# Performance work log

Hardware: AMD Instinct MI355X
Metric: run time of the kernel (lower is better)

## Reference

```python
import jax, jax.numpy as jnp
import numpy as np

D_MODEL = 1024
N_HEADS = 16
HEAD_DIM = D_MODEL // N_HEADS  # 64
LATENT = 256
B, S = 2, 2048


def setup_inputs() -> dict:
    key = jax.random.key(0)
    ks = jax.random.split(key, 13)
    sc = 0.02
    inp = {
        'x': jax.random.normal(ks[0], (B, S, D_MODEL), jnp.float32),
        'Wq': jax.random.normal(ks[1], (D_MODEL, D_MODEL), jnp.float32) * sc,
        'bq': jnp.zeros((D_MODEL,), jnp.float32),
        'Wkd': jax.random.normal(ks[2], (D_MODEL, LATENT), jnp.float32) * sc,
        'bkd': jnp.zeros((LATENT,), jnp.float32),
        'Wvd': jax.random.normal(ks[3], (D_MODEL, LATENT), jnp.float32) * sc,
        'bvd': jnp.zeros((LATENT,), jnp.float32),
        'Wku': jax.random.normal(ks[4], (LATENT, D_MODEL), jnp.float32) * sc,
        'bku': jnp.zeros((D_MODEL,), jnp.float32),
        'Wvu': jax.random.normal(ks[5], (LATENT, D_MODEL), jnp.float32) * sc,
        'bvu': jnp.zeros((D_MODEL,), jnp.float32),
        'Wo': jax.random.normal(ks[6], (D_MODEL, D_MODEL), jnp.float32) * sc,
        'bo': jnp.zeros((D_MODEL,), jnp.float32),
    }
    return inp


def reference(x, Wq, bq, Wkd, bkd, Wvd, bvd, Wku, bku, Wvu, bvu, Wo, bo):
    b, s, _ = x.shape
    # projections
    Q = x @ Wq + bq                      # [b, s, d_model]
    K_latent = x @ Wkd + bkd             # [b, s, latent]
    V_latent = x @ Wvd + bvd             # [b, s, latent]
    K = K_latent @ Wku + bku             # [b, s, d_model]
    V = V_latent @ Wvu + bvu             # [b, s, d_model]
    # split heads
    Qh = Q.reshape(b, s, N_HEADS, HEAD_DIM)
    Kh = K.reshape(b, s, N_HEADS, HEAD_DIM)
    Vh = V.reshape(b, s, N_HEADS, HEAD_DIM)
    scale = 1.0 / jnp.sqrt(jnp.asarray(HEAD_DIM, x.dtype))
    scores = jnp.einsum('bqhd,bkhd->bhqk', Qh, Kh) * scale  # [b,h,s,s]
    attn = jax.nn.softmax(scores, axis=-1)
    ctx = jnp.einsum('bhqk,bkhd->bqhd', attn, Vh).reshape(b, s, D_MODEL)
    out = ctx @ Wo + bo
    return out
```

## Files before the change

kernel.cpp:

```cpp
#include <hip/hip_runtime.h>
#include <hip/hip_bf16.h>
#include <cstddef>

#define B_SZ 2
#define SEQ  2048
#define DM   1024
#define NH   16
#define HD   64
#define LAT  256
#define MTOT (B_SZ*SEQ)
#define NQKV 1536
#define QSCALE 0.18033688011112042f

typedef short bf16x8 __attribute__((ext_vector_type(8)));
typedef float floatx4 __attribute__((ext_vector_type(4)));
typedef unsigned short u16;

#if __has_builtin(__builtin_amdgcn_exp2f)
#define EXP2(x) __builtin_amdgcn_exp2f(x)
#else
#define EXP2(x) exp2f(x)
#endif

__device__ __forceinline__ u16 f2bf(float f) {
  union { float f; unsigned u; } a; a.f = f;
  unsigned r = a.u + 0x7FFFu + ((a.u >> 16) & 1u);
  return (u16)(r >> 16);
}

__device__ __forceinline__ floatx4 mfma16(bf16x8 a, bf16x8 b, floatx4 c) {
  return __builtin_amdgcn_mfma_f32_16x16x32_bf16(a, b, c, 0, 0, 0);
}

__device__ __forceinline__ void load16(const u16* g, u16* l) {
  __builtin_amdgcn_global_load_lds((const __attribute__((address_space(1))) unsigned*)g,
                                   (__attribute__((address_space(3))) unsigned*)l, 16, 0, 0);
}

__device__ void transpose_tile(const float* __restrict__ W, u16* __restrict__ WT,
                               int K, int N, int k0, int n0, u16 (*t)[65]) {
  const int r = threadIdx.x >> 4;
  const int c4 = (threadIdx.x & 15) * 4;
#pragma unroll
  for (int s = 0; s < 4; s++) {
    int row = s * 16 + r;
    float4 v = *(const float4*)&W[(size_t)(k0 + row) * N + n0 + c4];
    t[row][c4 + 0] = f2bf(v.x); t[row][c4 + 1] = f2bf(v.y);
    t[row][c4 + 2] = f2bf(v.z); t[row][c4 + 3] = f2bf(v.w);
  }
  __syncthreads();
  const int r2 = threadIdx.x >> 2;
  const int c8 = (threadIdx.x & 3) * 16;
  __align__(16) u16 tmp[16];
#pragma unroll
  for (int i = 0; i < 16; i++) tmp[i] = t[c8 + i][r2];
  u16* dst = WT + (size_t)(n0 + r2) * K + k0 + c8;
  *(bf16x8*)dst       = *(const bf16x8*)&tmp[0];
  *(bf16x8*)(dst + 8) = *(const bf16x8*)&tmp[8];
}

__global__ __launch_bounds__(256)
void prep_k(const float* __restrict__ x, u16* __restrict__ xb,
            const float* __restrict__ Wq, const float* __restrict__ Wkd,
            const float* __restrict__ Wvd, const float* __restrict__ Wku,
            const float* __restrict__ Wvu, const float* __restrict__ Wo,
            u16* __restrict__ WstkT, u16* __restrict__ WkuT,
            u16* __restrict__ WvuT, u16* __restrict__ WoT,
            const float* __restrict__ bq, const float* __restrict__ bkd,
            const float* __restrict__ bvd, float* __restrict__ bqkv) {
  __shared__ u16 t[64][65];
  const int blk = blockIdx.x;
  if (blk < 4096) {
    int i = blk * 256 + threadIdx.x;
    float4 v = ((const float4*)x)[i];
    ushort4 o; o.x = f2bf(v.x); o.y = f2bf(v.y); o.z = f2bf(v.z); o.w = f2bf(v.w);
    ((ushort4*)xb)[i] = o;
  } else if (blk < 4352) {
    int tt = blk - 4096;
    transpose_tile(Wq, WstkT, DM, DM, (tt >> 4) * 64, (tt & 15) * 64, t);
  } else if (blk < 4416) {
    int tt = blk - 4352;
    transpose_tile(Wkd, WstkT + (size_t)DM * DM, DM, LAT, (tt >> 2) * 64, (tt & 3) * 64, t);
  } else if (blk < 4480) {
    int tt = blk - 4416;
    transpose_tile(Wvd, WstkT + (size_t)1280 * DM, DM, LAT, (tt >> 2) * 64, (tt & 3) * 64, t);
  } else if (blk < 4544) {
    int tt = blk - 4480;
    transpose_tile(Wku, WkuT, LAT, DM, (tt >> 4) * 64, (tt & 15) * 64, t);
  } else if (blk < 4608) {
    int tt = blk - 4544;
    transpose_tile(Wvu, WvuT, LAT, DM, (tt >> 4) * 64, (tt & 15) * 64, t);
  } else if (blk < 4864) {
    int tt = blk - 4608;
    transpose_tile(Wo, WoT, DM, DM, (tt >> 4) * 64, (tt & 15) * 64, t);
  } else {
    int i = (blk - 4864) * 256 + threadIdx.x;
    float v = (i < 1024) ? bq[i] : (i < 1280) ? bkd[i - 1024] : bvd[i - 1280];
    bqkv[i] = v;
  }
}

template<int TM, int OUT_BF16, int VT1>
__global__ __launch_bounds__(256)
void gemm_bt(const u16* __restrict__ A0, const u16* __restrict__ A1,
             const u16* __restrict__ BT0, const u16* __restrict__ BT1,
             const float* __restrict__ bias0, const float* __restrict__ bias1,
             void* __restrict__ C0, void* __restrict__ C1,
             int M, int N, int Kd, int lda, float qscale, int qcols) {
  constexpr int FM = TM / 32;
  __shared__ u16 As[TM * 64];
  __shared__ u16 Bs[64 * 64];
  const u16* A  = blockIdx.z ? A1 : A0;
  const u16* BT = blockIdx.z ? BT1 : BT0;
  const float* bias = blockIdx.z ? bias1 : bias0;
  void* C = blockIdx.z ? C1 : C0;

  const int tid = threadIdx.x;
  const int m0 = blockIdx.y * TM, n0 = blockIdx.x * 64;
  const int wave = tid >> 6, lane = tid & 63;
  const int l15 = lane & 15, quad = lane >> 4;
  const int wm = (wave >> 1) * (TM / 2), wn = (wave & 1) * 32;

  floatx4 acc[FM][2];
#pragma unroll
  for (int i = 0; i < FM; i++)
#pragma unroll
    for (int j = 0; j < 2; j++) acc[i][j] = (floatx4){0.f, 0.f, 0.f, 0.f};

  const int tr = tid >> 3;
  const int tc8 = (tid & 7) * 8;
  const u16* Ag = A  + (size_t)(m0 + tr) * lda + tc8;
  const u16* Bg = BT + (size_t)(n0 + tr) * Kd + tc8;
  u16* AsW = &As[(size_t)tid * 8];
  u16* BsW = &Bs[(size_t)tid * 8];

  for (int k0 = 0; k0 < Kd; k0 += 64) {
    __syncthreads();
#pragma unroll
    for (int s = 0; s < FM; s++)
      load16(Ag + (size_t)(s * 32) * lda + k0, AsW + s * 2048);
#pragma unroll
    for (int s = 0; s < 2; s++)
      load16(Bg + (size_t)(s * 32) * Kd  + k0, BsW + s * 2048);
    __syncthreads();
#pragma unroll
    for (int kk = 0; kk < 2; kk++) {
      bf16x8 af[FM], bfr[2];
#pragma unroll
      for (int i = 0; i < FM; i++)
        af[i]  = *(const bf16x8*)&As[(wm + i * 16 + l15) * 64 + kk * 32 + quad * 8];
#pragma unroll
      for (int j = 0; j < 2; j++)
        bfr[j] = *(const bf16x8*)&Bs[(wn + j * 16 + l15) * 64 + kk * 32 + quad * 8];
#pragma unroll
      for (int i = 0; i < FM; i++)
#pragma unroll
        for (int j = 0; j < 2; j++)
          acc[i][j] = mfma16(af[i], bfr[j], acc[i][j]);
    }
  }

  if (VT1 && blockIdx.z == 1) {
#pragma unroll
    for (int i = 0; i < FM; i++) {
      int row = m0 + wm + i * 16 + quad * 4;
      int bb = row >> 11, sb = row & 2047;
#pragma unroll
      for (int j = 0; j < 2; j++) {
        int col = n0 + wn + j * 16 + l15;
        float bv = bias[col];
        union { u16 u[4]; uint2 w2; } tv;
#pragma unroll
        for (int r = 0; r < 4; r++) tv.u[r] = f2bf(acc[i][j][r] + bv);
        *(uint2*)((u16*)C + ((size_t)(bb * 16 + (col >> 6)) * 64 + (col & 63)) * SEQ + sb) = tv.w2;
      }
    }
  } else {
#pragma unroll
    for (int i = 0; i < FM; i++) {
      int row = m0 + wm + i * 16 + quad * 4;
#pragma unroll
      for (int j = 0; j < 2; j++) {
        int col = n0 + wn + j * 16 + l15;
        float bv = bias[col];
        float sc = (col < qcols) ? qscale : 1.f;
#pragma unroll
        for (int r = 0; r < 4; r++) {
          float v = (acc[i][j][r] + bv) * sc;
          if (OUT_BF16) ((u16*)C)[(size_t)(row + r) * N + col] = f2bf(v);
          else          ((float*)C)[(size_t)(row + r) * N + col] = v;
        }
      }
    }
  }
}

__global__ __launch_bounds__(256, 2)
void attn_fused(const u16* __restrict__ Q, const u16* __restrict__ K,
                const u16* __restrict__ VT, u16* __restrict__ CTX) {
  __shared__ float Ocmb[64][68];
  __shared__ float Lw[4][64];
  __shared__ u16 Plds[4][2][64][40];
  const int lin = blockIdx.y * gridDim.x + blockIdx.x;
  const int idx = lin >> 3;
  const int bh = (lin & 7) * 4 + (idx >> 5);
  const int q0 = (idx & 31) * 64;
  const int b = bh >> 4, h = bh & 15;
  const int wave = threadIdx.x >> 6, lane = threadIdx.x & 63;
  const int l15 = lane & 15, quad = lane >> 4;

  bf16x8 qf[4][2];
  {
    const u16* Qp = Q + (size_t)(b * SEQ + q0 + l15) * NQKV + h * HD + quad * 8;
#pragma unroll
    for (int qi = 0; qi < 4; qi++)
#pragma unroll
      for (int h2 = 0; h2 < 2; h2++)
        qf[qi][h2] = *(const bf16x8*)(Qp + (size_t)qi * 16 * NQKV + h2 * 32);
  }
  const u16* Kp = K + (size_t)(b * SEQ) * DM + h * HD + quad * 8;
  const u16* Vp = VT + ((size_t)bh * HD + l15) * SEQ + quad * 8;

  floatx4 o[4][4];
#pragma unroll
  for (int dt = 0; dt < 4; dt++)
#pragma unroll
    for (int qi = 0; qi < 4; qi++) o[dt][qi] = (floatx4){0.f, 0.f, 0.f, 0.f};
  float ls[4] = {0.f, 0.f, 0.f, 0.f};

  const int kb0 = wave * 512;

  bf16x8 kfb[2][2][2], vfb[2][4];
#pragma unroll
  for (int ki = 0; ki < 2; ki++)
#pragma unroll
    for (int h2 = 0; h2 < 2; h2++)
      kfb[0][ki][h2] = *(const bf16x8*)(Kp + (size_t)(kb0 + ki * 16 + l15) * DM + h2 * 32);
#pragma unroll
  for (int dt = 0; dt < 4; dt++)
    vfb[0][dt] = *(const bf16x8*)(Vp + (size_t)(dt * 16) * SEQ + kb0);

#pragma unroll 2
  for (int it = 0; it < 16; ++it) {
    const int cur = it & 1, nxt = cur ^ 1;
    const int kb = kb0 + it * 32;
    if (it < 15) {
      const int kn = kb + 32;
#pragma unroll
      for (int ki = 0; ki < 2; ki++)
#pragma unroll
        for (int h2 = 0; h2 < 2; h2++)
          kfb[nxt][ki][h2] = *(const bf16x8*)(Kp + (size_t)(kn + ki * 16 + l15) * DM + h2 * 32);
    }
    __builtin_amdgcn_s_setprio(1);
    if (it > 0) {
#pragma unroll
      for (int qi = 0; qi < 4; qi++) {
        bf16x8 pf = *(const bf16x8*)&Plds[wave][nxt][qi * 16 + l15][quad * 8];
#pragma unroll
        for (int dt = 0; dt < 4; dt++)
          o[dt][qi] = mfma16(vfb[nxt][dt], pf, o[dt][qi]);
      }
    }
    if (it < 15) {
      const int kn = kb + 32;
#pragma unroll
      for (int dt = 0; dt < 4; dt++)
        vfb[nxt][dt] = *(const bf16x8*)(Vp + (size_t)(dt * 16) * SEQ + kn);
    }
    unsigned pw[4][4];
#pragma unroll
    for (int qi = 0; qi < 4; qi++) {
#pragma unroll
      for (int ki = 0; ki < 2; ki++) {
        floatx4 z = (floatx4){0.f, 0.f, 0.f, 0.f};
        z = mfma16(kfb[cur][ki][0], qf[qi][0], z);
        z = mfma16(kfb[cur][ki][1], qf[qi][1], z);
        float p0 = EXP2(z[0]), p1 = EXP2(z[1]), p2 = EXP2(z[2]), p3 = EXP2(z[3]);
        ls[qi] += (p0 + p1) + (p2 + p3);
        unsigned u0 = __float_as_uint(p0) + 0x8000u;
        unsigned u1 = __float_as_uint(p1) + 0x8000u;
        unsigned u2 = __float_as_uint(p2) + 0x8000u;
        unsigned u3 = __float_as_uint(p3) + 0x8000u;
        pw[qi][ki * 2]     = __builtin_amdgcn_perm(u1, u0, 0x07060302u);
        pw[qi][ki * 2 + 1] = __builtin_amdgcn_perm(u3, u2, 0x07060302u);
      }
    }
    __builtin_amdgcn_s_setprio(0);
#pragma unroll
    for (int qi = 0; qi < 4; qi++) {
      uint2 w0; w0.x = pw[qi][0]; w0.y = pw[qi][1];
      *(uint2*)&Plds[wave][cur][qi * 16 + l15][quad * 4] = w0;
      uint2 w1; w1.x = pw[qi][2]; w1.y = pw[qi][3];
      *(uint2*)&Plds[wave][cur][qi * 16 + l15][16 + quad * 4] = w1;
    }
  }
  __builtin_amdgcn_s_setprio(1);
#pragma unroll
  for (int qi = 0; qi < 4; qi++) {
    bf16x8 pf = *(const bf16x8*)&Plds[wave][1][qi * 16 + l15][quad * 8];
#pragma unroll
    for (int dt = 0; dt < 4; dt++)
      o[dt][qi] = mfma16(vfb[1][dt], pf, o[dt][qi]);
  }
  __builtin_amdgcn_s_setprio(0);

#pragma unroll
  for (int qi = 0; qi < 4; qi++) {
    float v = ls[qi];
    v += __shfl_xor(v, 16);
    v += __shfl_xor(v, 32);
    if (quad == 0) Lw[wave][qi * 16 + l15] = v;
  }
  if (wave == 0) {
#pragma unroll
    for (int dt = 0; dt < 4; dt++)
#pragma unroll
      for (int qi = 0; qi < 4; qi++)
        *(floatx4*)&Ocmb[qi * 16 + l15][dt * 16 + quad * 4] = o[dt][qi];
  }
  __syncthreads();
  if (wave == 1) {
#pragma unroll
    for (int dt = 0; dt < 4; dt++)
#pragma unroll
      for (int qi = 0; qi < 4; qi++) {
        floatx4* pp = (floatx4*)&Ocmb[qi * 16 + l15][dt * 16 + quad * 4];
        *pp = *pp + o[dt][qi];
      }
  }
  __syncthreads();
  if (wave == 2) {
#pragma unroll
    for (int dt = 0; dt < 4; dt++)
#pragma unroll
      for (int qi = 0; qi < 4; qi++) {
        floatx4* pp = (floatx4*)&Ocmb[qi * 16 + l15][dt * 16 + quad * 4];
        *pp = *pp + o[dt][qi];
      }
  }
  __syncthreads();
  if (wave == 3) {
#pragma unroll
    for (int qi = 0; qi < 4; qi++) {
      int qq = qi * 16 + l15;
      float lt = Lw[0][qq] + Lw[1][qq] + Lw[2][qq] + Lw[3][qq];
      float inv = 1.f / lt;
      u16* Crow = CTX + (size_t)(b * SEQ + q0 + qq) * DM + h * HD + quad * 4;
#pragma unroll
      for (int dt = 0; dt < 4; dt++) {
        floatx4 ov = o[dt][qi] + *(const floatx4*)&Ocmb[qq][dt * 16 + quad * 4];
        union { u16 u[4]; uint2 w2; } tv;
#pragma unroll
        for (int r = 0; r < 4; r++) tv.u[r] = f2bf(ov[r] * inv);
        *(uint2*)(Crow + dt * 16) = tv.w2;
      }
    }
  }
}

extern "C" void kernel_launch(void* const* d_in, const int* in_sizes, int n_in,
                              void* d_out, int out_size, void* d_ws, size_t ws_size,
                              hipStream_t stream) {
  const float* x   = (const float*)d_in[0];
  const float* Wq  = (const float*)d_in[1];
  const float* bq  = (const float*)d_in[2];
  const float* Wkd = (const float*)d_in[3];
  const float* bkd = (const float*)d_in[4];
  const float* Wvd = (const float*)d_in[5];
  const float* bvd = (const float*)d_in[6];
  const float* Wku = (const float*)d_in[7];
  const float* bku = (const float*)d_in[8];
  const float* Wvu = (const float*)d_in[9];
  const float* bvu = (const float*)d_in[10];
  const float* Wo  = (const float*)d_in[11];
  const float* bo  = (const float*)d_in[12];
  float* out = (float*)d_out;

  float* bqkv = (float*)d_ws;
  u16* p = (u16*)((char*)d_ws + 1536 * sizeof(float));
  u16* xb    = p; p += (size_t)MTOT * DM;
  u16* WstkT = p; p += (size_t)NQKV * DM;
  u16* WkuT  = p; p += (size_t)DM * LAT;
  u16* WvuT  = p; p += (size_t)DM * LAT;
  u16* WoT   = p; p += (size_t)DM * DM;
  u16* QKVb  = p; p += (size_t)MTOT * NQKV;
  u16* Kb    = p; p += (size_t)MTOT * DM;
  u16* VTb   = p; p += (size_t)MTOT * DM;
  u16* CXb   = p; p += (size_t)MTOT * DM;

  prep_k<<<4870, 256, 0, stream>>>(x, xb, Wq, Wkd, Wvd, Wku, Wvu, Wo,
                                   WstkT, WkuT, WvuT, WoT, bq, bkd, bvd, bqkv);

  gemm_bt<128, 1, 0><<<dim3(NQKV / 64, MTOT / 128, 1), 256, 0, stream>>>(
      xb, xb, WstkT, WstkT, bqkv, bqkv, QKVb, QKVb, MTOT, NQKV, DM, DM, QSCALE, DM);
  gemm_bt<128, 1, 1><<<dim3(DM / 64, MTOT / 128, 2), 256, 0, stream>>>(
      QKVb + 1024, QKVb + 1280, WkuT, WvuT, bku, bvu, Kb, VTb, MTOT, DM, LAT, NQKV, 1.f, 0);

  attn_fused<<<dim3(SEQ / 64, B_SZ * NH), 256, 0, stream>>>(QKVb, Kb, VTb, CXb);

  gemm_bt<64, 0, 0><<<dim3(DM / 64, MTOT / 64, 1), 256, 0, stream>>>(
      CXb, CXb, WoT, WoT, bo, bo, out, out, MTOT, DM, DM, DM, 1.f, 0);
}
```

Before: 224.0 us.

## Switch attention to 32x32x16 MFMA and pass P via lane shuffles instead of LDS

Rewrites the attention inner loop to use 32x32x16 bf16 MFMA tiles instead of 16x16x32, with matching fragment layouts for Q, K, V^T and the output accumulators. The probability tile is now repacked into B-operand form with cross-half-wave shuffles, which removes the per-wave LDS staging buffer and its store/load round trip. The aim is fewer MFMA issues, no LDS traffic in the hot loop, and a lighter epilogue. The cost is extra shuffles and selects per tile, and P·V now runs in the same iteration as QK^T, so the previous software pipelining between them is gone.

```diff
diff --git a/kernel.cpp b/kernel.cpp
--- a/kernel.cpp
+++ b/kernel.cpp
@@ -14,6 +14,7 @@
 
 typedef short bf16x8 __attribute__((ext_vector_type(8)));
 typedef float floatx4 __attribute__((ext_vector_type(4)));
+typedef float floatx16 __attribute__((ext_vector_type(16)));
 typedef unsigned short u16;
 
 #if __has_builtin(__builtin_amdgcn_exp2f)
@@ -30,6 +31,10 @@
 
 __device__ __forceinline__ floatx4 mfma16(bf16x8 a, bf16x8 b, floatx4 c) {
   return __builtin_amdgcn_mfma_f32_16x16x32_bf16(a, b, c, 0, 0, 0);
+}
+
+__device__ __forceinline__ floatx16 mfma32(bf16x8 a, bf16x8 b, floatx16 c) {
+  return __builtin_amdgcn_mfma_f32_32x32x16_bf16(a, b, c, 0, 0, 0);
 }
 
 __device__ __forceinline__ void load16(const u16* g, u16* l) {
@@ -200,45 +205,46 @@
                 const u16* __restrict__ VT, u16* __restrict__ CTX) {
   __shared__ float Ocmb[64][68];
   __shared__ float Lw[4][64];
-  __shared__ u16 Plds[4][2][64][40];
   const int lin = blockIdx.y * gridDim.x + blockIdx.x;
   const int idx = lin >> 3;
   const int bh = (lin & 7) * 4 + (idx >> 5);
   const int q0 = (idx & 31) * 64;
   const int b = bh >> 4, h = bh & 15;
   const int wave = threadIdx.x >> 6, lane = threadIdx.x & 63;
-  const int l15 = lane & 15, quad = lane >> 4;
-
-  bf16x8 qf[4][2];
+  const int l31 = lane & 31;
+  const int hi = lane >> 5;
+
+  bf16x8 qf[2][4];
   {
-    const u16* Qp = Q + (size_t)(b * SEQ + q0 + l15) * NQKV + h * HD + quad * 8;
-#pragma unroll
-    for (int qi = 0; qi < 4; qi++)
-#pragma unroll
-      for (int h2 = 0; h2 < 2; h2++)
-        qf[qi][h2] = *(const bf16x8*)(Qp + (size_t)qi * 16 * NQKV + h2 * 32);
-  }
-  const u16* Kp = K + (size_t)(b * SEQ) * DM + h * HD + quad * 8;
-  const u16* Vp = VT + ((size_t)bh * HD + l15) * SEQ + quad * 8;
-
-  floatx4 o[4][4];
-#pragma unroll
-  for (int dt = 0; dt < 4; dt++)
-#pragma unroll
-    for (int qi = 0; qi < 4; qi++) o[dt][qi] = (floatx4){0.f, 0.f, 0.f, 0.f};
-  float ls[4] = {0.f, 0.f, 0.f, 0.f};
+    const u16* Qp = Q + (size_t)(b * SEQ + q0 + l31) * NQKV + h * HD + hi * 8;
+#pragma unroll
+    for (int qh = 0; qh < 2; qh++)
+#pragma unroll
+      for (int dc = 0; dc < 4; dc++)
+        qf[qh][dc] = *(const bf16x8*)(Qp + (size_t)(qh * 32) * NQKV + dc * 16);
+  }
+  const u16* Kp = K + ((size_t)(b * SEQ) + l31) * DM + h * HD + hi * 8;
+  const u16* Vp = VT + ((size_t)bh * HD + l31) * SEQ + hi * 8;
+
+  floatx16 o[2][2];
+  const floatx16 zf16 = {0.f,0.f,0.f,0.f,0.f,0.f,0.f,0.f,0.f,0.f,0.f,0.f,0.f,0.f,0.f,0.f};
+#pragma unroll
+  for (int dh = 0; dh < 2; dh++)
+#pragma unroll
+    for (int qh = 0; qh < 2; qh++) o[dh][qh] = zf16;
+  float ls[2] = {0.f, 0.f};
 
   const int kb0 = wave * 512;
 
-  bf16x8 kfb[2][2][2], vfb[2][4];
-#pragma unroll
-  for (int ki = 0; ki < 2; ki++)
-#pragma unroll
-    for (int h2 = 0; h2 < 2; h2++)
-      kfb[0][ki][h2] = *(const bf16x8*)(Kp + (size_t)(kb0 + ki * 16 + l15) * DM + h2 * 32);
-#pragma unroll
-  for (int dt = 0; dt < 4; dt++)
-    vfb[0][dt] = *(const bf16x8*)(Vp + (size_t)(dt * 16) * SEQ + kb0);
+  bf16x8 kfb[2][4], vfb[2][2][2];
+#pragma unroll
+  for (int dc = 0; dc < 4; dc++)
+    kfb[0][dc] = *(const bf16x8*)(Kp + (size_t)kb0 * DM + dc * 16);
+#pragma unroll
+  for (int dh = 0; dh < 2; dh++)
+#pragma unroll
+    for (int kh = 0; kh < 2; kh++)
+      vfb[0][dh][kh] = *(const bf16x8*)(Vp + (size_t)(dh * 32) * SEQ + kb0 + kh * 16);
 
 #pragma unroll 2
   for (int it = 0; it < 16; ++it) {
@@ -247,114 +253,121 @@
     if (it < 15) {
       const int kn = kb + 32;
 #pragma unroll
-      for (int ki = 0; ki < 2; ki++)
-#pragma unroll
-        for (int h2 = 0; h2 < 2; h2++)
-          kfb[nxt][ki][h2] = *(const bf16x8*)(Kp + (size_t)(kn + ki * 16 + l15) * DM + h2 * 32);
-    }
-    __builtin_amdgcn_s_setprio(1);
-    if (it > 0) {
-#pragma unroll
-      for (int qi = 0; qi < 4; qi++) {
-        bf16x8 pf = *(const bf16x8*)&Plds[wave][nxt][qi * 16 + l15][quad * 8];
-#pragma unroll
-        for (int dt = 0; dt < 4; dt++)
-          o[dt][qi] = mfma16(vfb[nxt][dt], pf, o[dt][qi]);
+      for (int dc = 0; dc < 4; dc++)
+        kfb[nxt][dc] = *(const bf16x8*)(Kp + (size_t)kn * DM + dc * 16);
+#pragma unroll
+      for (int dh = 0; dh < 2; dh++)
+#pragma unroll
+        for (int kh = 0; kh < 2; kh++)
+          vfb[nxt][dh][kh] = *(const bf16x8*)(Vp + (size_t)(dh * 32) * SEQ + kn + kh * 16);
+    }
+#pragma unroll
+    for (int qh = 0; qh < 2; qh++) {
+      floatx16 z = zf16;
+      __builtin_amdgcn_s_setprio(1);
+#pragma unroll
+      for (int dc = 0; dc < 4; dc++)
+        z = mfma32(kfb[cur][dc], qf[qh][dc], z);
+      __builtin_amdgcn_s_setprio(0);
+      float p[16];
+#pragma unroll
+      for (int r = 0; r < 16; r++) p[r] = EXP2(z[r]);
+      ls[qh] += (((p[0] + p[1]) + (p[2] + p[3])) + ((p[4] + p[5]) + (p[6] + p[7])))
+              + (((p[8] + p[9]) + (p[10] + p[11])) + ((p[12] + p[13]) + (p[14] + p[15])));
+      unsigned wt[8];
+#pragma unroll
+      for (int i = 0; i < 8; i++) {
+        unsigned ua = __float_as_uint(p[2 * i]) + 0x8000u;
+        unsigned ub = __float_as_uint(p[2 * i + 1]) + 0x8000u;
+        wt[i] = __builtin_amdgcn_perm(ub, ua, 0x07060302u);
       }
-    }
-    if (it < 15) {
-      const int kn = kb + 32;
-#pragma unroll
-      for (int dt = 0; dt < 4; dt++)
-        vfb[nxt][dt] = *(const bf16x8*)(Vp + (size_t)(dt * 16) * SEQ + kn);
-    }
-    unsigned pw[4][4];
-#pragma unroll
-    for (int qi = 0; qi < 4; qi++) {
-#pragma unroll
-      for (int ki = 0; ki < 2; ki++) {
-        floatx4 z = (floatx4){0.f, 0.f, 0.f, 0.f};
-        z = mfma16(kfb[cur][ki][0], qf[qi][0], z);
-        z = mfma16(kfb[cur][ki][1], qf[qi][1], z);
-        float p0 = EXP2(z[0]), p1 = EXP2(z[1]), p2 = EXP2(z[2]), p3 = EXP2(z[3]);
-        ls[qi] += (p0 + p1) + (p2 + p3);
-        unsigned u0 = __float_as_uint(p0) + 0x8000u;
-        unsigned u1 = __float_as_uint(p1) + 0x8000u;
-        unsigned u2 = __float_as_uint(p2) + 0x8000u;
-        unsigned u3 = __float_as_uint(p3) + 0x8000u;
-        pw[qi][ki * 2]     = __builtin_amdgcn_perm(u1, u0, 0x07060302u);
-        pw[qi][ki * 2 + 1] = __builtin_amdgcn_perm(u3, u2, 0x07060302u);
+      unsigned sx[8];
+#pragma unroll
+      for (int i = 0; i < 8; i++) sx[i] = (unsigned)__shfl_xor((int)wt[i], 32);
+      union { unsigned u[4]; bf16x8 v; } b0, b1;
+      b0.u[0] = hi ? sx[2] : wt[0];
+      b0.u[1] = hi ? sx[3] : wt[1];
+      b0.u[2] = hi ? wt[2] : sx[0];
+      b0.u[3] = hi ? wt[3] : sx[1];
+      b1.u[0] = hi ? sx[6] : wt[4];
+      b1.u[1] = hi ? sx[7] : wt[5];
+      b1.u[2] = hi ? wt[6] : sx[4];
+      b1.u[3] = hi ? wt[7] : sx[5];
+      __builtin_amdgcn_s_setprio(1);
+#pragma unroll
+      for (int dh = 0; dh < 2; dh++) {
+        o[dh][qh] = mfma32(vfb[cur][dh][0], b0.v, o[dh][qh]);
+        o[dh][qh] = mfma32(vfb[cur][dh][1], b1.v, o[dh][qh]);
       }
-    }
-    __builtin_amdgcn_s_setprio(0);
-#pragma unroll
-    for (int qi = 0; qi < 4; qi++) {
-      uint2 w0; w0.x = pw[qi][0]; w0.y = pw[qi][1];
-      *(uint2*)&Plds[wave][cur][qi * 16 + l15][quad * 4] = w0;
-      uint2 w1; w1.x = pw[qi][2]; w1.y = pw[qi][3];
-      *(uint2*)&Plds[wave][cur][qi * 16 + l15][16 + quad * 4] = w1;
-    }
-  }
-  __builtin_amdgcn_s_setprio(1);
-#pragma unroll
-  for (int qi = 0; qi < 4; qi++) {
-    bf16x8 pf = *(const bf16x8*)&Plds[wave][1][qi * 16 + l15][quad * 8];
-#pragma unroll
-    for (int dt = 0; dt < 4; dt++)
-      o[dt][qi] = mfma16(vfb[1][dt], pf, o[dt][qi]);
-  }
-  __builtin_amdgcn_s_setprio(0);
-
-#pragma unroll
-  for (int qi = 0; qi < 4; qi++) {
-    float v = ls[qi];
-    v += __shfl_xor(v, 16);
+      __builtin_amdgcn_s_setprio(0);
+    }
+  }
+
+#pragma unroll
+  for (int qh = 0; qh < 2; qh++) {
+    float v = ls[qh];
     v += __shfl_xor(v, 32);
-    if (quad == 0) Lw[wave][qi * 16 + l15] = v;
+    if (hi == 0) Lw[wave][qh * 32 + l31] = v;
   }
   if (wave == 0) {
 #pragma unroll
-    for (int dt = 0; dt < 4; dt++)
-#pragma unroll
-      for (int qi = 0; qi < 4; qi++)
-        *(floatx4*)&Ocmb[qi * 16 + l15][dt * 16 + quad * 4] = o[dt][qi];
+    for (int dh = 0; dh < 2; dh++)
+#pragma unroll
+      for (int qh = 0; qh < 2; qh++)
+#pragma unroll
+        for (int g = 0; g < 4; g++) {
+          floatx4 t = {o[dh][qh][4 * g], o[dh][qh][4 * g + 1],
+                       o[dh][qh][4 * g + 2], o[dh][qh][4 * g + 3]};
+          *(floatx4*)&Ocmb[qh * 32 + l31][dh * 32 + g * 8 + hi * 4] = t;
+        }
   }
   __syncthreads();
   if (wave == 1) {
 #pragma unroll
-    for (int dt = 0; dt < 4; dt++)
-#pragma unroll
-      for (int qi = 0; qi < 4; qi++) {
-        floatx4* pp = (floatx4*)&Ocmb[qi * 16 + l15][dt * 16 + quad * 4];
-        *pp = *pp + o[dt][qi];
-      }
+    for (int dh = 0; dh < 2; dh++)
+#pragma unroll
+      for (int qh = 0; qh < 2; qh++)
+#pragma unroll
+        for (int g = 0; g < 4; g++) {
+          floatx4* pp = (floatx4*)&Ocmb[qh * 32 + l31][dh * 32 + g * 8 + hi * 4];
+          floatx4 t = {o[dh][qh][4 * g], o[dh][qh][4 * g + 1],
+                       o[dh][qh][4 * g + 2], o[dh][qh][4 * g + 3]};
+          *pp = *pp + t;
+        }
   }
   __syncthreads();
   if (wave == 2) {
 #pragma unroll
-    for (int dt = 0; dt < 4; dt++)
-#pragma unroll
-      for (int qi = 0; qi < 4; qi++) {
-        floatx4* pp = (floatx4*)&Ocmb[qi * 16 + l15][dt * 16 + quad * 4];
-        *pp = *pp + o[dt][qi];
-      }
+    for (int dh = 0; dh < 2; dh++)
+#pragma unroll
+      for (int qh = 0; qh < 2; qh++)
+#pragma unroll
+        for (int g = 0; g < 4; g++) {
+          floatx4* pp = (floatx4*)&Ocmb[qh * 32 + l31][dh * 32 + g * 8 + hi * 4];
+          floatx4 t = {o[dh][qh][4 * g], o[dh][qh][4 * g + 1],
+                       o[dh][qh][4 * g + 2], o[dh][qh][4 * g + 3]};
+          *pp = *pp + t;
+        }
   }
   __syncthreads();
   if (wave == 3) {
 #pragma unroll
-    for (int qi = 0; qi < 4; qi++) {
-      int qq = qi * 16 + l15;
+    for (int qh = 0; qh < 2; qh++) {
+      int qq = qh * 32 + l31;
       float lt = Lw[0][qq] + Lw[1][qq] + Lw[2][qq] + Lw[3][qq];
       float inv = 1.f / lt;
-      u16* Crow = CTX + (size_t)(b * SEQ + q0 + qq) * DM + h * HD + quad * 4;
-#pragma unroll
-      for (int dt = 0; dt < 4; dt++) {
-        floatx4 ov = o[dt][qi] + *(const floatx4*)&Ocmb[qq][dt * 16 + quad * 4];
-        union { u16 u[4]; uint2 w2; } tv;
-#pragma unroll
-        for (int r = 0; r < 4; r++) tv.u[r] = f2bf(ov[r] * inv);
-        *(uint2*)(Crow + dt * 16) = tv.w2;
-      }
+      u16* Crow = CTX + (size_t)(b * SEQ + q0 + qq) * DM + h * HD + hi * 4;
+#pragma unroll
+      for (int dh = 0; dh < 2; dh++)
+#pragma unroll
+        for (int g = 0; g < 4; g++) {
+          const float* oc = &Ocmb[qq][dh * 32 + g * 8 + hi * 4];
+          union { u16 u[4]; uint2 w2; } tv;
+#pragma unroll
+          for (int r = 0; r < 4; r++)
+            tv.u[r] = f2bf((o[dh][qh][4 * g + r] + oc[r]) * inv);
+          *(uint2*)(Crow + dh * 32 + g * 8) = tv.w2;
+        }
     }
   }
 }
```

After: 224.7 us. No clear change (+0.3%).
